# Kernel tuning notes

Measured on AMD Instinct MI355X. Metric: run time of the kernel, lower is better.

## Reference

```python
import jax, jax.numpy as jnp
import numpy as np

N = 50000      # nodes
E = 800000     # edges (avg degree 16)
DIN = 500      # input_dim
HID = 100      # hid_dim (fixed in module)
DOUT = 64      # output_dim
EPS = 1e-5     # LayerNorm eps (torch default)


def _layer_norm(x, g, b):
    mu = jnp.mean(x, axis=-1, keepdims=True)
    var = jnp.var(x, axis=-1, keepdims=True)
    return (x - mu) / jnp.sqrt(var + EPS) * g + b


def _gcn_conv(x, src, tgt, W, b):
    # PyG GCNConv: self-loops + symmetric normalization + linear + scatter-add
    h = x @ W  # [N, out]
    idx = jnp.arange(N)
    src_sl = jnp.concatenate([src, idx])
    tgt_sl = jnp.concatenate([tgt, idx])
    deg = jax.ops.segment_sum(jnp.ones(src_sl.shape, h.dtype), tgt_sl, num_segments=N)
    dinv = jnp.where(deg > 0, deg ** -0.5, 0.0)
    norm = dinv[src_sl] * dinv[tgt_sl]  # [E+N]
    out = jax.ops.segment_sum(h[src_sl] * norm[:, None], tgt_sl, num_segments=N)
    return out + b


def setup_inputs() -> dict:
    key = jax.random.key(0)
    ks = jax.random.split(key, 10)
    glorot = lambda k, fi, fo: jax.random.normal(k, (fi, fo), jnp.float32) * np.float32(1.0 / np.sqrt(fi))
    z = lambda d: jnp.zeros((d,), jnp.float32)
    return dict(
        data_x=jax.random.normal(ks[0], (N, DIN), jnp.float32),
        data_edge_index=jax.random.randint(ks[1], (2, E), 0, N),
        data_edge_attr=jnp.zeros((E,), jnp.int32),  # single relation type
        t_W1=glorot(ks[2], DIN, HID), t_b1=z(HID), t_g1=jnp.ones((HID,), jnp.float32), t_be1=z(HID),
        t_W2=glorot(ks[3], HID, HID), t_b2=z(HID), t_g2=jnp.ones((HID,), jnp.float32), t_be2=z(HID),
        r_Wrel=glorot(ks[4], HID, HID)[None],  # [n_relations=1, H, H]
        r_Wself=glorot(ks[5], HID, HID), r_b=z(HID),
        c1_W=glorot(ks[6], HID, HID), c1_b=z(HID),
        c2_W=glorot(ks[7], HID, DOUT), c2_b=z(DOUT),
    )


def reference(data_x, data_edge_index, data_edge_attr,
              t_W1, t_b1, t_g1, t_be1, t_W2, t_b2, t_g2, t_be2,
              r_Wrel, r_Wself, r_b, c1_W, c1_b, c2_W, c2_b):
    src, tgt = data_edge_index[0], data_edge_index[1]
    # transform: Linear -> LN -> ReLU -> Linear -> LN -> ReLU
    x = jax.nn.relu(_layer_norm(data_x @ t_W1 + t_b1, t_g1, t_be1))
    x = jax.nn.relu(_layer_norm(x @ t_W2 + t_b2, t_g2, t_be2))
    # RGCN, n_relations=1, n_layers=1: per-relation message + self transform
    msgs = x[src] @ r_Wrel[0]  # edge_attr is all relation 0
    x = x @ r_Wself + jax.ops.segment_sum(msgs, tgt, num_segments=N) + r_b
    x = jax.nn.relu(x)  # dropout = identity (eval)
    x = jax.nn.relu(_gcn_conv(x, src, tgt, c1_W, c1_b))
    x = _gcn_conv(x, src, tgt, c2_W, c2_b)
    return jax.nn.log_softmax(x, axis=1)
```

## Files before the change

kernel.cpp:

```cpp
#include <hip/hip_runtime.h>
#include <hip/hip_bf16.h>

typedef __attribute__((ext_vector_type(8))) short short8;
typedef __attribute__((ext_vector_type(8))) unsigned short ushort8;
typedef __attribute__((ext_vector_type(4))) float f32x4;

static constexpr int NN = 50000;
static constexpr int NE = 800000;
static constexpr int SCAN_B = 196;

#define MFMA16x16x32 __builtin_amdgcn_mfma_f32_16x16x32_bf16

__device__ __forceinline__ float b2f(unsigned short u){
  unsigned v = ((unsigned)u) << 16;
  return __builtin_bit_cast(float, v);
}
__device__ __forceinline__ unsigned short f2b(float f){
  unsigned x = __builtin_bit_cast(unsigned, f);
  unsigned r = (x + 0x7fffu + ((x >> 16) & 1u)) >> 16;
  return (unsigned short)r;
}

__device__ __align__(256) int   g_isf32;
__device__ __align__(256) unsigned short g_W1t  [112 * 512];
__device__ __align__(256) unsigned short g_W2t  [112 * 128];
__device__ __align__(256) unsigned short g_WselfT[112 * 128];
__device__ __align__(256) unsigned short g_WrelT [112 * 128];
__device__ __align__(256) unsigned short g_c1Wt [112 * 128];
__device__ __align__(256) unsigned short g_c2Wt [64 * 128];
__device__ __align__(256) unsigned short g_bufA[(size_t)NN * 128];
__device__ __align__(256) unsigned short g_bufB[(size_t)NN * 128];
__device__ __align__(256) unsigned short g_bufC[(size_t)NN * 128];
__device__ __align__(256) int   g_deg[NN];
__device__ __align__(256) int   g_rowptr[NN + 1];
__device__ __align__(256) int   g_cursor[NN];
__device__ __align__(256) int   g_colidx[NE];
__device__ __align__(256) float g_dinv[NN];
__device__ __align__(256) int   g_partial[256];

__device__ __forceinline__ float ld_in(const void* p, int idx, int isf32){
  if (isf32) return ((const float*)p)[idx];
  return b2f(((const unsigned short*)p)[idx]);
}

__global__ void k_detect_zero(const unsigned short* __restrict__ x){
  if (blockIdx.x == 0){
    __shared__ int sh[256];
    int tid = threadIdx.x;
    int cnt = 0;
    for (int j = 0; j < 16; j++){
      unsigned short h = x[(size_t)(tid * 16 + j) * 2];
      int e = (h >> 7) & 0xFF;
      if (e >= 90 && e <= 160) cnt++;
    }
    sh[tid] = cnt;
    __syncthreads();
    for (int off = 128; off > 0; off >>= 1){
      if (tid < off) sh[tid] += sh[tid + off];
      __syncthreads();
    }
    if (tid == 0) g_isf32 = (sh[0] < 2458) ? 1 : 0;
  } else {
    int i = (blockIdx.x - 1) * 256 + threadIdx.x;
    if (i < NN){ g_deg[i] = 0; g_cursor[i] = 0; }
  }
}

__device__ __forceinline__ void xp_one(const void* W, unsigned short* Wt, int idx,
                                       int K, int Nc, int Kpad, int isf32){
  int n = idx / Kpad;
  int k = idx - n * Kpad;
  float v = 0.f;
  if (n < Nc && k < K) v = ld_in(W, k * Nc + n, isf32);
  Wt[idx] = f2b(v);
}
__global__ void k_transpose_all(const void* W1, const void* W2, const void* Wself,
                                const void* Wrel, const void* c1W, const void* c2W){
  int idx = blockIdx.x * 256 + threadIdx.x;
  const int isf32 = g_isf32;
  if (idx < 57344){ xp_one(W1, g_W1t, idx, 500, 100, 512, isf32); return; }
  idx -= 57344;
  if (idx < 14336){ xp_one(W2,    g_W2t,    idx, 100, 100, 128, isf32); return; }
  idx -= 14336;
  if (idx < 14336){ xp_one(Wself, g_WselfT, idx, 100, 100, 128, isf32); return; }
  idx -= 14336;
  if (idx < 14336){ xp_one(Wrel,  g_WrelT,  idx, 100, 100, 128, isf32); return; }
  idx -= 14336;
  if (idx < 14336){ xp_one(c1W,   g_c1Wt,   idx, 100, 100, 128, isf32); return; }
  idx -= 14336;
  if (idx < 8192){  xp_one(c2W,   g_c2Wt,   idx, 100, 64,  128, isf32); }
}

__global__ void k_deg(const int* __restrict__ tgt){
  int e = blockIdx.x * 256 + threadIdx.x;
  if (e < NE) atomicAdd(&g_deg[tgt[e]], 1);
}
__global__ __launch_bounds__(256) void k_scan1(){
  __shared__ int sh[256];
  int t = threadIdx.x;
  int i = blockIdx.x * 256 + t;
  int val = (i < NN) ? g_deg[i] : 0;
  sh[t] = val; __syncthreads();
#pragma unroll
  for (int off = 1; off < 256; off <<= 1){
    int v = (t >= off) ? sh[t - off] : 0;
    __syncthreads(); sh[t] += v; __syncthreads();
  }
  if (i < NN){ g_rowptr[i] = sh[t] - val; g_dinv[i] = rsqrtf((float)(val + 1)); }
  if (t == 255) g_partial[blockIdx.x] = sh[255];
}
__global__ __launch_bounds__(256) void k_scan2(){
  __shared__ int sh[256];
  int t = threadIdx.x;
  int val = (t < SCAN_B) ? g_partial[t] : 0;
  sh[t] = val; __syncthreads();
#pragma unroll
  for (int off = 1; off < 256; off <<= 1){
    int v = (t >= off) ? sh[t - off] : 0;
    __syncthreads(); sh[t] += v; __syncthreads();
  }
  if (t < SCAN_B) g_partial[t] = sh[t] - val;
  if (t == 255) g_rowptr[NN] = sh[255];
}
__global__ __launch_bounds__(256) void k_scan3(){
  int i = blockIdx.x * 256 + threadIdx.x;
  if (i < NN) g_rowptr[i] += g_partial[blockIdx.x];
}
__global__ void k_fill(const int* __restrict__ src, const int* __restrict__ tgt){
  int e = blockIdx.x * 256 + threadIdx.x;
  if (e >= NE) return;
  int t = tgt[e];
  int pos = g_rowptr[t] + atomicAdd(&g_cursor[t], 1);
  g_colidx[pos] = src[e];
}


__device__ __forceinline__ void body_gemm1_compute(const void* Aext, int row0,
    int m, int q, int kbase, int isf32, f32x4* acc){
  if (isf32){
    const float* base = (const float*)Aext + (size_t)(row0 + m) * 500;
    f32x4 L[8];
#pragma unroll
    for (int c = 0; c < 4; c++){
      int col = kbase + c * 32 + q * 8;
      L[2 * c]     = *reinterpret_cast<const f32x4*>(base + min(col, 496));
      L[2 * c + 1] = *reinterpret_cast<const f32x4*>(base + min(col + 4, 496));
    }
#pragma unroll
    for (int c = 0; c < 4; c++){
      f32x4 lo = L[2 * c], hi = L[2 * c + 1];
      short8 a = {(short)f2b(lo[0]), (short)f2b(lo[1]), (short)f2b(lo[2]), (short)f2b(lo[3]),
                  (short)f2b(hi[0]), (short)f2b(hi[1]), (short)f2b(hi[2]), (short)f2b(hi[3])};
      const int k0 = kbase + c * 32 + q * 8;
#pragma unroll
      for (int t = 0; t < 7; t++){
        short8 b = *reinterpret_cast<const short8*>(g_W1t + (size_t)(t * 16 + m) * 512 + k0);
        acc[t] = MFMA16x16x32(a, b, acc[t], 0, 0, 0);
      }
    }
  } else {
    const unsigned short* base = (const unsigned short*)Aext + (size_t)(row0 + m) * 500;
    ushort4 U[8];
#pragma unroll
    for (int c = 0; c < 4; c++){
      int col = kbase + c * 32 + q * 8;
      U[2 * c]     = *reinterpret_cast<const ushort4*>(base + min(col, 496));
      U[2 * c + 1] = *reinterpret_cast<const ushort4*>(base + min(col + 4, 496));
    }
#pragma unroll
    for (int c = 0; c < 4; c++){
      ushort4 lo = U[2 * c], hi = U[2 * c + 1];
      short8 a = {(short)lo.x, (short)lo.y, (short)lo.z, (short)lo.w,
                  (short)hi.x, (short)hi.y, (short)hi.z, (short)hi.w};
      const int k0 = kbase + c * 32 + q * 8;
#pragma unroll
      for (int t = 0; t < 7; t++){
        short8 b = *reinterpret_cast<const short8*>(g_W1t + (size_t)(t * 16 + m) * 512 + k0);
        acc[t] = MFMA16x16x32(a, b, acc[t], 0, 0, 0);
      }
    }
  }
}

__device__ __forceinline__ short8 frag_from_lds(const float* xT, int m, int k0){
  const float* ax = xT + m * 132 + k0;
  short8 a = {(short)f2b(ax[0]), (short)f2b(ax[1]), (short)f2b(ax[2]), (short)f2b(ax[3]),
              (short)f2b(ax[4]), (short)f2b(ax[5]), (short)f2b(ax[6]), (short)f2b(ax[7])};
  return a;
}

__device__ __forceinline__ void epi_ln_to_lds(const float* red, float* xT,
    int lane, int m, int q, int isf32,
    const void* bias, const void* gamma, const void* beta){
  float bf_[7], gf_[7], ef_[7];
#pragma unroll
  for (int t = 0; t < 7; t++){
    int col = t * 16 + m;
    bool ok = col < 100;
    bf_[t] = ok ? ld_in(bias, col, isf32)  : 0.f;
    gf_[t] = ok ? ld_in(gamma, col, isf32) : 0.f;
    ef_[t] = ok ? ld_in(beta, col, isf32)  : 0.f;
  }
#pragma unroll
  for (int r = 0; r < 4; r++){
    float vals[7], s1 = 0.f, s2 = 0.f;
#pragma unroll
    for (int t = 0; t < 7; t++){
      const float* rv = &red[(t * 4 + r) * 256];
      float v = rv[lane] + rv[64 + lane] + rv[128 + lane] + rv[192 + lane];
      int col = t * 16 + m;
      v = (col < 100) ? (v + bf_[t]) : 0.f;
      vals[t] = v; s1 += v; s2 += v * v;
    }
#pragma unroll
    for (int msk = 1; msk < 16; msk <<= 1){
      s1 += __shfl_xor(s1, msk, 64);
      s2 += __shfl_xor(s2, msk, 64);
    }
    float mu = s1 * 0.01f;
    float var = fmaxf(s2 * 0.01f - mu * mu, 0.f);
    float rstd = rsqrtf(var + 1e-5f);
    float* xrow = xT + (q * 4 + r) * 132;
#pragma unroll
    for (int t = 0; t < 7; t++){
      int col = t * 16 + m;
      float y = fmaxf((vals[t] - mu) * rstd * gf_[t] + ef_[t], 0.f);
      xrow[col] = (col < 100) ? y : 0.f;
    }
    xrow[112 + m] = 0.f;
  }
}

__device__ __forceinline__ void epi_ln_to_global(const float* red, unsigned short* outb,
    int row0, int lane, int m, int q, int isf32,
    const void* bias, const void* gamma, const void* beta){
  float bf_[7], gf_[7], ef_[7];
#pragma unroll
  for (int t = 0; t < 7; t++){
    int col = t * 16 + m;
    bool ok = col < 100;
    bf_[t] = ok ? ld_in(bias, col, isf32)  : 0.f;
    gf_[t] = ok ? ld_in(gamma, col, isf32) : 0.f;
    ef_[t] = ok ? ld_in(beta, col, isf32)  : 0.f;
  }
#pragma unroll
  for (int r = 0; r < 4; r++){
    float vals[7], s1 = 0.f, s2 = 0.f;
#pragma unroll
    for (int t = 0; t < 7; t++){
      const float* rv = &red[(t * 4 + r) * 256];
      float v = rv[lane] + rv[64 + lane] + rv[128 + lane] + rv[192 + lane];
      int col = t * 16 + m;
      v = (col < 100) ? (v + bf_[t]) : 0.f;
      vals[t] = v; s1 += v; s2 += v * v;
    }
#pragma unroll
    for (int msk = 1; msk < 16; msk <<= 1){
      s1 += __shfl_xor(s1, msk, 64);
      s2 += __shfl_xor(s2, msk, 64);
    }
    float mu = s1 * 0.01f;
    float var = fmaxf(s2 * 0.01f - mu * mu, 0.f);
    float rstd = rsqrtf(var + 1e-5f);
    unsigned short* orow = outb + (size_t)(row0 + q * 4 + r) * 128;
#pragma unroll
    for (int t = 0; t < 7; t++){
      int col = t * 16 + m;
      float y = fmaxf((vals[t] - mu) * rstd * gf_[t] + ef_[t], 0.f);
      orow[col] = f2b((col < 100) ? y : 0.f);
    }
    orow[112 + m] = 0;
  }
}

__device__ __forceinline__ void epi_biasrelu_to_global(const float* red,
    unsigned short* outb, int row0, int lane, int m, int q, int isf32,
    const void* bias){
  float bf_[7];
#pragma unroll
  for (int t = 0; t < 7; t++){
    int col = t * 16 + m;
    bf_[t] = (col < 100) ? ld_in(bias, col, isf32) : 0.f;
  }
#pragma unroll
  for (int r = 0; r < 4; r++){
    unsigned short* orow = outb + (size_t)(row0 + q * 4 + r) * 128;
#pragma unroll
    for (int t = 0; t < 7; t++){
      const float* rv = &red[(t * 4 + r) * 256];
      float v = rv[lane] + rv[64 + lane] + rv[128 + lane] + rv[192 + lane];
      int col = t * 16 + m;
      float y = fmaxf(v + bf_[t], 0.f);
      orow[col] = f2b((col < 100) ? y : 0.f);
    }
    orow[112 + m] = 0;
  }
}

__device__ __forceinline__ void epi_biasrelu_to_lds(const float* red, float* xT,
    int lane, int m, int q, int isf32, const void* bias){
  float bf_[7];
#pragma unroll
  for (int t = 0; t < 7; t++){
    int col = t * 16 + m;
    bf_[t] = (col < 100) ? ld_in(bias, col, isf32) : 0.f;
  }
#pragma unroll
  for (int r = 0; r < 4; r++){
    float* xrow = xT + (q * 4 + r) * 132;
#pragma unroll
    for (int t = 0; t < 7; t++){
      const float* rv = &red[(t * 4 + r) * 256];
      float v = rv[lane] + rv[64 + lane] + rv[128 + lane] + rv[192 + lane];
      int col = t * 16 + m;
      float y = fmaxf(v + bf_[t], 0.f);
      xrow[col] = (col < 100) ? y : 0.f;
    }
    xrow[112 + m] = 0.f;
  }
}

template<int MODE>
__device__ __forceinline__ void agg_to_lds(int node, int nl, int c8, float* aggT){
  const unsigned short* x = (MODE == 1) ? g_bufC : g_bufB;
  float wt = (MODE != 0) ? g_dinv[node] : 1.f;
  float a[4][8];
#pragma unroll
  for (int j = 0; j < 4; j++)
#pragma unroll
    for (int k = 0; k < 8; k++) a[j][k] = 0.f;
  int p0 = g_rowptr[node], p1 = g_rowptr[node + 1];
  for (int p = p0; p < p1; p += 4){
    int sj[4]; float wj[4];
#pragma unroll
    for (int j = 0; j < 4; j++){
      bool ok = (p + j) < p1;
      sj[j] = ok ? g_colidx[p + j] : node;
      wj[j] = ok ? ((MODE != 0) ? g_dinv[sj[j]] * wt : 1.f) : 0.f;
    }
    ushort8 r[4];
#pragma unroll
    for (int j = 0; j < 4; j++)
      r[j] = *reinterpret_cast<const ushort8*>(&x[(size_t)sj[j] * 128 + c8]);
#pragma unroll
    for (int j = 0; j < 4; j++)
#pragma unroll
      for (int k = 0; k < 8; k++) a[j][k] += wj[j] * b2f((unsigned short)r[j][k]);
  }
  if (MODE != 0){
    float ws = wt * wt;
    ushort8 sv = *reinterpret_cast<const ushort8*>(&x[(size_t)node * 128 + c8]);
#pragma unroll
    for (int k = 0; k < 8; k++) a[0][k] += ws * b2f((unsigned short)sv[k]);
  }
  float* arow = aggT + nl * 132;
#pragma unroll
  for (int k = 0; k < 8; k++)
    arow[c8 + k] = a[0][k] + a[1][k] + a[2][k] + a[3][k];
}


__global__ __launch_bounds__(256, 4) void k_gemm12(const void* __restrict__ Aext,
    const void* b1, const void* gm1, const void* be1,
    const void* b2, const void* gm2, const void* be2){
  __shared__ float red[28 * 256];
  __shared__ float xT[16 * 132];
  const int tid = threadIdx.x;
  const int w = tid >> 6, lane = tid & 63;
  const int m = lane & 15, q = lane >> 4;
  const int row0 = blockIdx.x * 16;
  const int isf32 = g_isf32;

  f32x4 acc[7] = {};
  body_gemm1_compute(Aext, row0, m, q, w * 128, isf32, acc);
#pragma unroll
  for (int t = 0; t < 7; t++)
#pragma unroll
    for (int r = 0; r < 4; r++)
      red[(t * 4 + r) * 256 + tid] = acc[t][r];
  __syncthreads();
  if (w == 0) epi_ln_to_lds(red, xT, lane, m, q, isf32, b1, gm1, be1);
  __syncthreads();

  f32x4 acc2[7] = {};
  const int k0 = w * 32 + q * 8;
  {
    short8 a = frag_from_lds(xT, m, k0);
#pragma unroll
    for (int t = 0; t < 7; t++){
      short8 b = *reinterpret_cast<const short8*>(g_W2t + (size_t)(t * 16 + m) * 128 + k0);
      acc2[t] = MFMA16x16x32(a, b, acc2[t], 0, 0, 0);
    }
  }
#pragma unroll
  for (int t = 0; t < 7; t++)
#pragma unroll
    for (int r = 0; r < 4; r++)
      red[(t * 4 + r) * 256 + tid] = acc2[t][r];
  __syncthreads();
  if (w == 0) epi_ln_to_global(red, g_bufB, row0, lane, m, q, isf32, b2, gm2, be2);
}

__global__ __launch_bounds__(256, 4) void k_rgcn_f(const void* rb){
  __shared__ float red[28 * 256];
  __shared__ float aggT[16 * 132];
  const int tid = threadIdx.x;
  agg_to_lds<0>(blockIdx.x * 16 + (tid >> 4), tid >> 4, (tid & 15) * 8, aggT);
  __syncthreads();

  const int w = tid >> 6, lane = tid & 63;
  const int m = lane & 15, q = lane >> 4;
  const int row0 = blockIdx.x * 16;
  const int k0 = w * 32 + q * 8;
  f32x4 acc[7] = {};
  {
    short8 a1 = *reinterpret_cast<const short8*>(g_bufB + (size_t)(row0 + m) * 128 + k0);
#pragma unroll
    for (int t = 0; t < 7; t++){
      short8 b = *reinterpret_cast<const short8*>(g_WselfT + (size_t)(t * 16 + m) * 128 + k0);
      acc[t] = MFMA16x16x32(a1, b, acc[t], 0, 0, 0);
    }
    short8 a2 = frag_from_lds(aggT, m, k0);
#pragma unroll
    for (int t = 0; t < 7; t++){
      short8 b = *reinterpret_cast<const short8*>(g_WrelT + (size_t)(t * 16 + m) * 128 + k0);
      acc[t] = MFMA16x16x32(a2, b, acc[t], 0, 0, 0);
    }
  }
#pragma unroll
  for (int t = 0; t < 7; t++)
#pragma unroll
    for (int r = 0; r < 4; r++)
      red[(t * 4 + r) * 256 + tid] = acc[t][r];
  __syncthreads();
  if (w == 0) epi_biasrelu_to_global(red, g_bufC, row0, lane, m, q, g_isf32, rb);
}

__global__ __launch_bounds__(256, 4) void k_conv_f(const void* c1b){
  __shared__ float red[28 * 256];
  __shared__ float aggT[16 * 132];
  const int tid = threadIdx.x;
  agg_to_lds<1>(blockIdx.x * 16 + (tid >> 4), tid >> 4, (tid & 15) * 8, aggT);
  __syncthreads();

  const int w = tid >> 6, lane = tid & 63;
  const int m = lane & 15, q = lane >> 4;
  const int row0 = blockIdx.x * 16;
  const int k0 = w * 32 + q * 8;
  f32x4 acc[7] = {};
  {
    short8 a = frag_from_lds(aggT, m, k0);
#pragma unroll
    for (int t = 0; t < 7; t++){
      short8 b = *reinterpret_cast<const short8*>(g_c1Wt + (size_t)(t * 16 + m) * 128 + k0);
      acc[t] = MFMA16x16x32(a, b, acc[t], 0, 0, 0);
    }
  }
#pragma unroll
  for (int t = 0; t < 7; t++)
#pragma unroll
    for (int r = 0; r < 4; r++)
      red[(t * 4 + r) * 256 + tid] = acc[t][r];
  __syncthreads();
  if (w == 0) epi_biasrelu_to_lds(red, aggT, lane, m, q, g_isf32, c1b);
  __syncthreads();

  f32x4 acc2[4] = {};
  {
    short8 a = frag_from_lds(aggT, m, k0);
#pragma unroll
    for (int t = 0; t < 4; t++){
      short8 b = *reinterpret_cast<const short8*>(g_c2Wt + (size_t)(t * 16 + m) * 128 + k0);
      acc2[t] = MFMA16x16x32(a, b, acc2[t], 0, 0, 0);
    }
  }
#pragma unroll
  for (int t = 0; t < 4; t++)
#pragma unroll
    for (int r = 0; r < 4; r++)
      red[(t * 4 + r) * 256 + tid] = acc2[t][r];
  __syncthreads();
  if (w == 0){
#pragma unroll
    for (int r = 0; r < 4; r++){
      unsigned short* orow = g_bufA + (size_t)(row0 + q * 4 + r) * 64;
#pragma unroll
      for (int t = 0; t < 4; t++){
        const float* rv = &red[(t * 4 + r) * 256];
        float v = rv[lane] + rv[64 + lane] + rv[128 + lane] + rv[192 + lane];
        orow[t * 16 + m] = f2b(v);
      }
    }
  }
}

__global__ __launch_bounds__(256) void k_agg_lsm(const void* __restrict__ bias,
                                                 void* __restrict__ outv){
  const int isf32 = g_isf32;
  int node = blockIdx.x * 32 + (threadIdx.x >> 3);
  if (node >= NN) return;
  const int c8 = (threadIdx.x & 7) * 8;
  float wt = g_dinv[node];
  float a[4][8];
#pragma unroll
  for (int j = 0; j < 4; j++)
#pragma unroll
    for (int k = 0; k < 8; k++) a[j][k] = 0.f;
  int p0 = g_rowptr[node], p1 = g_rowptr[node + 1];
  for (int p = p0; p < p1; p += 4){
    int sj[4]; float wj[4];
#pragma unroll
    for (int j = 0; j < 4; j++){
      bool ok = (p + j) < p1;
      sj[j] = ok ? g_colidx[p + j] : node;
      wj[j] = ok ? g_dinv[sj[j]] * wt : 0.f;
    }
    ushort8 r[4];
#pragma unroll
    for (int j = 0; j < 4; j++)
      r[j] = *reinterpret_cast<const ushort8*>(&g_bufA[(size_t)sj[j] * 64 + c8]);
#pragma unroll
    for (int j = 0; j < 4; j++)
#pragma unroll
      for (int k = 0; k < 8; k++) a[j][k] += wj[j] * b2f((unsigned short)r[j][k]);
  }
  float ws = wt * wt;
  ushort8 sv = *reinterpret_cast<const ushort8*>(&g_bufA[(size_t)node * 64 + c8]);
#pragma unroll
  for (int k = 0; k < 8; k++) a[0][k] += ws * b2f((unsigned short)sv[k]);

  float v[8], mx = -1e30f;
#pragma unroll
  for (int k = 0; k < 8; k++){
    v[k] = a[0][k] + a[1][k] + a[2][k] + a[3][k] + ld_in(bias, c8 + k, isf32);
    mx = fmaxf(mx, v[k]);
  }
#pragma unroll
  for (int msk = 1; msk < 8; msk <<= 1) mx = fmaxf(mx, __shfl_xor(mx, msk, 64));
  float se = 0.f;
#pragma unroll
  for (int k = 0; k < 8; k++) se += expf(v[k] - mx);
#pragma unroll
  for (int msk = 1; msk < 8; msk <<= 1) se += __shfl_xor(se, msk, 64);
  float lse = logf(se);
  size_t ro = (size_t)node * 64 + c8;
  if (isf32){
    float* o = (float*)outv + ro;
#pragma unroll
    for (int k = 0; k < 8; k++) o[k] = v[k] - mx - lse;
  } else {
    unsigned short* o = (unsigned short*)outv + ro;
#pragma unroll
    for (int k = 0; k < 8; k++) o[k] = f2b(v[k] - mx - lse);
  }
}

extern "C" void kernel_launch(void* const* d_in, const int* in_sizes, int n_in,
                              void* d_out, int out_size, void* d_ws, size_t ws_size,
                              hipStream_t stream){
  (void)in_sizes; (void)n_in; (void)out_size; (void)d_ws; (void)ws_size;
  const void* data_x = d_in[0];
  const int* ei = (const int*)d_in[1];
  const int* src = ei;
  const int* tgt = ei + NE;
  const void *W1 = d_in[3], *b1 = d_in[4], *gm1 = d_in[5], *be1 = d_in[6];
  const void *W2 = d_in[7], *b2 = d_in[8], *gm2 = d_in[9], *be2 = d_in[10];
  const void *Wrel = d_in[11], *Wself = d_in[12], *rb = d_in[13];
  const void *c1W = d_in[14], *c1b = d_in[15];
  const void *c2W = d_in[16], *c2b = d_in[17];

  k_detect_zero<<<1 + (NN + 255) / 256, 256, 0, stream>>>((const unsigned short*)data_x);
  k_transpose_all<<<(122880 + 255) / 256, 256, 0, stream>>>(W1, W2, Wself, Wrel, c1W, c2W);

  k_deg<<<(NE + 255) / 256, 256, 0, stream>>>(tgt);
  k_scan1<<<SCAN_B, 256, 0, stream>>>();
  k_scan2<<<1, 256, 0, stream>>>();
  k_scan3<<<SCAN_B, 256, 0, stream>>>();
  k_fill<<<(NE + 255) / 256, 256, 0, stream>>>(src, tgt);

  k_gemm12<<<3125, 256, 0, stream>>>(data_x, b1, gm1, be1, b2, gm2, be2);
  k_rgcn_f<<<3125, 256, 0, stream>>>(rb);
  k_conv_f<<<3125, 256, 0, stream>>>(c1b);
  k_agg_lsm<<<(NN + 31) / 32, 256, 0, stream>>>(c2b, d_out);
}
```

Measured before the change: 487.3 us.

## Give each wave its own 16-row tile, dropping split-K LDS reduction

The three fused GEMM kernels now give each of the 4 waves its own 16-row tile and run the full K loop per wave, instead of splitting K across waves. This removes the 28x256 float LDS reduction buffer and the single-wave epilogue. Epilogues (bias, LayerNorm, ReLU) now run per wave directly on MFMA accumulators. Aggregation tiles are stored in LDS as bf16 rather than float, with 32 columns per thread and two neighbours per loop step. The block count drops to NBLK with row-bound guards, which adds register pressure per wave and changes the gather access pattern.

```diff
diff --git a/kernel.cpp b/kernel.cpp
--- a/kernel.cpp
+++ b/kernel.cpp
@@ -8,6 +8,7 @@
 static constexpr int NN = 50000;
 static constexpr int NE = 800000;
 static constexpr int SCAN_B = 196;
+static constexpr int NBLK = (NN + 63) / 64;
 
 #define MFMA16x16x32 __builtin_amdgcn_mfma_f32_16x16x32_bf16
 
@@ -19,6 +20,9 @@
   unsigned x = __builtin_bit_cast(unsigned, f);
   unsigned r = (x + 0x7fffu + ((x >> 16) & 1u)) >> 16;
   return (unsigned short)r;
+}
+__device__ __forceinline__ short8 u2s(ushort8 v){
+  return __builtin_bit_cast(short8, v);
 }
 
 __device__ __align__(256) int   g_isf32;
@@ -135,339 +139,235 @@
 }
 
 
-__device__ __forceinline__ void body_gemm1_compute(const void* Aext, int row0,
-    int m, int q, int kbase, int isf32, f32x4* acc){
-  if (isf32){
-    const float* base = (const float*)Aext + (size_t)(row0 + m) * 500;
-    f32x4 L[8];
-#pragma unroll
-    for (int c = 0; c < 4; c++){
-      int col = kbase + c * 32 + q * 8;
-      L[2 * c]     = *reinterpret_cast<const f32x4*>(base + min(col, 496));
-      L[2 * c + 1] = *reinterpret_cast<const f32x4*>(base + min(col + 4, 496));
-    }
-#pragma unroll
-    for (int c = 0; c < 4; c++){
-      f32x4 lo = L[2 * c], hi = L[2 * c + 1];
-      short8 a = {(short)f2b(lo[0]), (short)f2b(lo[1]), (short)f2b(lo[2]), (short)f2b(lo[3]),
-                  (short)f2b(hi[0]), (short)f2b(hi[1]), (short)f2b(hi[2]), (short)f2b(hi[3])};
-      const int k0 = kbase + c * 32 + q * 8;
-#pragma unroll
-      for (int t = 0; t < 7; t++){
-        short8 b = *reinterpret_cast<const short8*>(g_W1t + (size_t)(t * 16 + m) * 512 + k0);
-        acc[t] = MFMA16x16x32(a, b, acc[t], 0, 0, 0);
-      }
-    }
-  } else {
-    const unsigned short* base = (const unsigned short*)Aext + (size_t)(row0 + m) * 500;
-    ushort4 U[8];
-#pragma unroll
-    for (int c = 0; c < 4; c++){
-      int col = kbase + c * 32 + q * 8;
-      U[2 * c]     = *reinterpret_cast<const ushort4*>(base + min(col, 496));
-      U[2 * c + 1] = *reinterpret_cast<const ushort4*>(base + min(col + 4, 496));
-    }
-#pragma unroll
-    for (int c = 0; c < 4; c++){
-      ushort4 lo = U[2 * c], hi = U[2 * c + 1];
-      short8 a = {(short)lo.x, (short)lo.y, (short)lo.z, (short)lo.w,
-                  (short)hi.x, (short)hi.y, (short)hi.z, (short)hi.w};
-      const int k0 = kbase + c * 32 + q * 8;
-#pragma unroll
-      for (int t = 0; t < 7; t++){
-        short8 b = *reinterpret_cast<const short8*>(g_W1t + (size_t)(t * 16 + m) * 512 + k0);
-        acc[t] = MFMA16x16x32(a, b, acc[t], 0, 0, 0);
-      }
-    }
-  }
-}
-
-__device__ __forceinline__ short8 frag_from_lds(const float* xT, int m, int k0){
-  const float* ax = xT + m * 132 + k0;
-  short8 a = {(short)f2b(ax[0]), (short)f2b(ax[1]), (short)f2b(ax[2]), (short)f2b(ax[3]),
-              (short)f2b(ax[4]), (short)f2b(ax[5]), (short)f2b(ax[6]), (short)f2b(ax[7])};
-  return a;
-}
-
-__device__ __forceinline__ void epi_ln_to_lds(const float* red, float* xT,
-    int lane, int m, int q, int isf32,
-    const void* bias, const void* gamma, const void* beta){
+template<int DO_LN>
+__device__ __forceinline__ void wave_epi(const f32x4* acc, unsigned short* dst,
+    int rstride, int grow0, int lane, int isf32,
+    const void* bias, const void* gm, const void* be){
+  const int m = lane & 15;
+  const int q = lane >> 4;
   float bf_[7], gf_[7], ef_[7];
 #pragma unroll
   for (int t = 0; t < 7; t++){
     int col = t * 16 + m;
     bool ok = col < 100;
-    bf_[t] = ok ? ld_in(bias, col, isf32)  : 0.f;
-    gf_[t] = ok ? ld_in(gamma, col, isf32) : 0.f;
-    ef_[t] = ok ? ld_in(beta, col, isf32)  : 0.f;
+    bf_[t] = ok ? ld_in(bias, col, isf32) : 0.f;
+    if (DO_LN){
+      gf_[t] = ok ? ld_in(gm, col, isf32) : 0.f;
+      ef_[t] = ok ? ld_in(be, col, isf32) : 0.f;
+    }
   }
 #pragma unroll
   for (int r = 0; r < 4; r++){
+    int rl = q * 4 + r;
     float vals[7], s1 = 0.f, s2 = 0.f;
-#pragma unroll
-    for (int t = 0; t < 7; t++){
-      const float* rv = &red[(t * 4 + r) * 256];
-      float v = rv[lane] + rv[64 + lane] + rv[128 + lane] + rv[192 + lane];
-      int col = t * 16 + m;
-      v = (col < 100) ? (v + bf_[t]) : 0.f;
-      vals[t] = v; s1 += v; s2 += v * v;
-    }
-#pragma unroll
-    for (int msk = 1; msk < 16; msk <<= 1){
-      s1 += __shfl_xor(s1, msk, 64);
-      s2 += __shfl_xor(s2, msk, 64);
-    }
-    float mu = s1 * 0.01f;
-    float var = fmaxf(s2 * 0.01f - mu * mu, 0.f);
-    float rstd = rsqrtf(var + 1e-5f);
-    float* xrow = xT + (q * 4 + r) * 132;
 #pragma unroll
     for (int t = 0; t < 7; t++){
       int col = t * 16 + m;
-      float y = fmaxf((vals[t] - mu) * rstd * gf_[t] + ef_[t], 0.f);
-      xrow[col] = (col < 100) ? y : 0.f;
-    }
-    xrow[112 + m] = 0.f;
-  }
-}
-
-__device__ __forceinline__ void epi_ln_to_global(const float* red, unsigned short* outb,
-    int row0, int lane, int m, int q, int isf32,
-    const void* bias, const void* gamma, const void* beta){
-  float bf_[7], gf_[7], ef_[7];
-#pragma unroll
-  for (int t = 0; t < 7; t++){
-    int col = t * 16 + m;
-    bool ok = col < 100;
-    bf_[t] = ok ? ld_in(bias, col, isf32)  : 0.f;
-    gf_[t] = ok ? ld_in(gamma, col, isf32) : 0.f;
-    ef_[t] = ok ? ld_in(beta, col, isf32)  : 0.f;
-  }
-#pragma unroll
-  for (int r = 0; r < 4; r++){
-    float vals[7], s1 = 0.f, s2 = 0.f;
-#pragma unroll
-    for (int t = 0; t < 7; t++){
-      const float* rv = &red[(t * 4 + r) * 256];
-      float v = rv[lane] + rv[64 + lane] + rv[128 + lane] + rv[192 + lane];
-      int col = t * 16 + m;
-      v = (col < 100) ? (v + bf_[t]) : 0.f;
+      float v = (col < 100) ? (acc[t][r] + bf_[t]) : 0.f;
       vals[t] = v; s1 += v; s2 += v * v;
     }
-#pragma unroll
-    for (int msk = 1; msk < 16; msk <<= 1){
-      s1 += __shfl_xor(s1, msk, 64);
-      s2 += __shfl_xor(s2, msk, 64);
-    }
-    float mu = s1 * 0.01f;
-    float var = fmaxf(s2 * 0.01f - mu * mu, 0.f);
-    float rstd = rsqrtf(var + 1e-5f);
-    unsigned short* orow = outb + (size_t)(row0 + q * 4 + r) * 128;
-#pragma unroll
-    for (int t = 0; t < 7; t++){
-      int col = t * 16 + m;
-      float y = fmaxf((vals[t] - mu) * rstd * gf_[t] + ef_[t], 0.f);
-      orow[col] = f2b((col < 100) ? y : 0.f);
-    }
-    orow[112 + m] = 0;
-  }
-}
-
-__device__ __forceinline__ void epi_biasrelu_to_global(const float* red,
-    unsigned short* outb, int row0, int lane, int m, int q, int isf32,
-    const void* bias){
-  float bf_[7];
-#pragma unroll
-  for (int t = 0; t < 7; t++){
-    int col = t * 16 + m;
-    bf_[t] = (col < 100) ? ld_in(bias, col, isf32) : 0.f;
-  }
-#pragma unroll
-  for (int r = 0; r < 4; r++){
-    unsigned short* orow = outb + (size_t)(row0 + q * 4 + r) * 128;
-#pragma unroll
-    for (int t = 0; t < 7; t++){
-      const float* rv = &red[(t * 4 + r) * 256];
-      float v = rv[lane] + rv[64 + lane] + rv[128 + lane] + rv[192 + lane];
-      int col = t * 16 + m;
-      float y = fmaxf(v + bf_[t], 0.f);
-      orow[col] = f2b((col < 100) ? y : 0.f);
-    }
-    orow[112 + m] = 0;
-  }
-}
-
-__device__ __forceinline__ void epi_biasrelu_to_lds(const float* red, float* xT,
-    int lane, int m, int q, int isf32, const void* bias){
-  float bf_[7];
-#pragma unroll
-  for (int t = 0; t < 7; t++){
-    int col = t * 16 + m;
-    bf_[t] = (col < 100) ? ld_in(bias, col, isf32) : 0.f;
-  }
-#pragma unroll
-  for (int r = 0; r < 4; r++){
-    float* xrow = xT + (q * 4 + r) * 132;
-#pragma unroll
-    for (int t = 0; t < 7; t++){
-      const float* rv = &red[(t * 4 + r) * 256];
-      float v = rv[lane] + rv[64 + lane] + rv[128 + lane] + rv[192 + lane];
-      int col = t * 16 + m;
-      float y = fmaxf(v + bf_[t], 0.f);
-      xrow[col] = (col < 100) ? y : 0.f;
-    }
-    xrow[112 + m] = 0.f;
+    if (DO_LN){
+#pragma unroll
+      for (int msk = 1; msk < 16; msk <<= 1){
+        s1 += __shfl_xor(s1, msk, 64);
+        s2 += __shfl_xor(s2, msk, 64);
+      }
+      float mu = s1 * 0.01f;
+      float var = fmaxf(s2 * 0.01f - mu * mu, 0.f);
+      float rstd = rsqrtf(var + 1e-5f);
+#pragma unroll
+      for (int t = 0; t < 7; t++)
+        vals[t] = (vals[t] - mu) * rstd * gf_[t] + ef_[t];
+    }
+    if (grow0 + rl < NN){
+      unsigned short* orow = dst + (size_t)rl * rstride;
+#pragma unroll
+      for (int t = 0; t < 7; t++){
+        int col = t * 16 + m;
+        float y = fmaxf(vals[t], 0.f);
+        orow[col] = f2b((col < 100) ? y : 0.f);
+      }
+      orow[112 + m] = 0;
+    }
   }
 }
 
 template<int MODE>
-__device__ __forceinline__ void agg_to_lds(int node, int nl, int c8, float* aggT){
-  const unsigned short* x = (MODE == 1) ? g_bufC : g_bufB;
-  float wt = (MODE != 0) ? g_dinv[node] : 1.f;
-  float a[4][8];
-#pragma unroll
-  for (int j = 0; j < 4; j++)
-#pragma unroll
-    for (int k = 0; k < 8; k++) a[j][k] = 0.f;
-  int p0 = g_rowptr[node], p1 = g_rowptr[node + 1];
-  for (int p = p0; p < p1; p += 4){
-    int sj[4]; float wj[4];
-#pragma unroll
-    for (int j = 0; j < 4; j++){
-      bool ok = (p + j) < p1;
-      sj[j] = ok ? g_colidx[p + j] : node;
-      wj[j] = ok ? ((MODE != 0) ? g_dinv[sj[j]] * wt : 1.f) : 0.f;
-    }
-    ushort8 r[4];
-#pragma unroll
-    for (int j = 0; j < 4; j++)
-      r[j] = *reinterpret_cast<const ushort8*>(&x[(size_t)sj[j] * 128 + c8]);
-#pragma unroll
-    for (int j = 0; j < 4; j++)
-#pragma unroll
-      for (int k = 0; k < 8; k++) a[j][k] += wj[j] * b2f((unsigned short)r[j][k]);
+__device__ __forceinline__ void agg_tile(const unsigned short* __restrict__ x,
+    unsigned short* aggT, int tid, int brow0){
+  const int nl = tid >> 2;
+  const int c0 = (tid & 3) * 32;
+  const int node = min(brow0 + nl, NN - 1);
+  const float wt = (MODE != 0) ? g_dinv[node] : 1.f;
+  float a[32];
+#pragma unroll
+  for (int k = 0; k < 32; k++) a[k] = 0.f;
+  const int p0 = g_rowptr[node], p1 = g_rowptr[node + 1];
+  for (int p = p0; p < p1; p += 2){
+    int s0 = g_colidx[p];
+    bool ok1 = (p + 1) < p1;
+    int s1 = ok1 ? g_colidx[p + 1] : node;
+    float w0 = (MODE != 0) ? g_dinv[s0] * wt : 1.f;
+    float w1 = ok1 ? ((MODE != 0) ? g_dinv[s1] * wt : 1.f) : 0.f;
+    ushort8 r0[4], r1[4];
+#pragma unroll
+    for (int u = 0; u < 4; u++){
+      r0[u] = *reinterpret_cast<const ushort8*>(&x[(size_t)s0 * 128 + c0 + u * 8]);
+      r1[u] = *reinterpret_cast<const ushort8*>(&x[(size_t)s1 * 128 + c0 + u * 8]);
+    }
+#pragma unroll
+    for (int u = 0; u < 4; u++)
+#pragma unroll
+      for (int k = 0; k < 8; k++){
+        a[u * 8 + k] += w0 * b2f((unsigned short)r0[u][k]);
+        a[u * 8 + k] += w1 * b2f((unsigned short)r1[u][k]);
+      }
   }
   if (MODE != 0){
     float ws = wt * wt;
-    ushort8 sv = *reinterpret_cast<const ushort8*>(&x[(size_t)node * 128 + c8]);
-#pragma unroll
-    for (int k = 0; k < 8; k++) a[0][k] += ws * b2f((unsigned short)sv[k]);
-  }
-  float* arow = aggT + nl * 132;
-#pragma unroll
-  for (int k = 0; k < 8; k++)
-    arow[c8 + k] = a[0][k] + a[1][k] + a[2][k] + a[3][k];
+#pragma unroll
+    for (int u = 0; u < 4; u++){
+      ushort8 sv = *reinterpret_cast<const ushort8*>(&x[(size_t)node * 128 + c0 + u * 8]);
+#pragma unroll
+      for (int k = 0; k < 8; k++) a[u * 8 + k] += ws * b2f((unsigned short)sv[k]);
+    }
+  }
+  unsigned short* arow = aggT + nl * 136 + c0;
+#pragma unroll
+  for (int u = 0; u < 4; u++){
+    ushort8 o;
+#pragma unroll
+    for (int k = 0; k < 8; k++) o[k] = f2b(a[u * 8 + k]);
+    *reinterpret_cast<ushort8*>(&arow[u * 8]) = o;
+  }
 }
 
 
 __global__ __launch_bounds__(256, 4) void k_gemm12(const void* __restrict__ Aext,
     const void* b1, const void* gm1, const void* be1,
     const void* b2, const void* gm2, const void* be2){
-  __shared__ float red[28 * 256];
-  __shared__ float xT[16 * 132];
+  __shared__ unsigned short xT[4][16][136];
   const int tid = threadIdx.x;
   const int w = tid >> 6, lane = tid & 63;
   const int m = lane & 15, q = lane >> 4;
-  const int row0 = blockIdx.x * 16;
+  const int row0 = blockIdx.x * 64 + w * 16;
   const int isf32 = g_isf32;
+  const int arow = min(row0 + m, NN - 1);
 
   f32x4 acc[7] = {};
-  body_gemm1_compute(Aext, row0, m, q, w * 128, isf32, acc);
-#pragma unroll
-  for (int t = 0; t < 7; t++)
-#pragma unroll
-    for (int r = 0; r < 4; r++)
-      red[(t * 4 + r) * 256 + tid] = acc[t][r];
+  if (isf32){
+    const float* base = (const float*)Aext + (size_t)arow * 500;
+#pragma unroll 4
+    for (int kc = 0; kc < 16; kc++){
+      int col = kc * 32 + q * 8;
+      f32x4 lo = *reinterpret_cast<const f32x4*>(base + min(col, 496));
+      f32x4 hi = *reinterpret_cast<const f32x4*>(base + min(col + 4, 496));
+      short8 a = {(short)f2b(lo[0]), (short)f2b(lo[1]), (short)f2b(lo[2]), (short)f2b(lo[3]),
+                  (short)f2b(hi[0]), (short)f2b(hi[1]), (short)f2b(hi[2]), (short)f2b(hi[3])};
+#pragma unroll
+      for (int t = 0; t < 7; t++){
+        short8 b = *reinterpret_cast<const short8*>(g_W1t + (size_t)(t * 16 + m) * 512 + col);
+        acc[t] = MFMA16x16x32(a, b, acc[t], 0, 0, 0);
+      }
+    }
+  } else {
+    const unsigned short* base = (const unsigned short*)Aext + (size_t)arow * 500;
+#pragma unroll 4
+    for (int kc = 0; kc < 16; kc++){
+      int col = kc * 32 + q * 8;
+      ushort4 lo = *reinterpret_cast<const ushort4*>(base + min(col, 496));
+      ushort4 hi = *reinterpret_cast<const ushort4*>(base + min(col + 4, 496));
+      short8 a = {(short)lo.x, (short)lo.y, (short)lo.z, (short)lo.w,
+                  (short)hi.x, (short)hi.y, (short)hi.z, (short)hi.w};
+#pragma unroll
+      for (int t = 0; t < 7; t++){
+        short8 b = *reinterpret_cast<const short8*>(g_W1t + (size_t)(t * 16 + m) * 512 + col);
+        acc[t] = MFMA16x16x32(a, b, acc[t], 0, 0, 0);
+      }
+    }
+  }
+  wave_epi<1>(acc, &xT[w][0][0], 136, 0, lane, isf32, b1, gm1, be1);
   __syncthreads();
-  if (w == 0) epi_ln_to_lds(red, xT, lane, m, q, isf32, b1, gm1, be1);
-  __syncthreads();
 
   f32x4 acc2[7] = {};
-  const int k0 = w * 32 + q * 8;
-  {
-    short8 a = frag_from_lds(xT, m, k0);
+#pragma unroll
+  for (int kc = 0; kc < 4; kc++){
+    int k0 = kc * 32 + q * 8;
+    short8 a = u2s(*reinterpret_cast<const ushort8*>(&xT[w][m][k0]));
 #pragma unroll
     for (int t = 0; t < 7; t++){
       short8 b = *reinterpret_cast<const short8*>(g_W2t + (size_t)(t * 16 + m) * 128 + k0);
       acc2[t] = MFMA16x16x32(a, b, acc2[t], 0, 0, 0);
     }
   }
-#pragma unroll
-  for (int t = 0; t < 7; t++)
-#pragma unroll
-    for (int r = 0; r < 4; r++)
-      red[(t * 4 + r) * 256 + tid] = acc2[t][r];
-  __syncthreads();
-  if (w == 0) epi_ln_to_global(red, g_bufB, row0, lane, m, q, isf32, b2, gm2, be2);
+  wave_epi<1>(acc2, g_bufB + (size_t)row0 * 128, 128, row0, lane, isf32, b2, gm2, be2);
 }
 
 __global__ __launch_bounds__(256, 4) void k_rgcn_f(const void* rb){
-  __shared__ float red[28 * 256];
-  __shared__ float aggT[16 * 132];
+  __shared__ unsigned short aggT[64 * 136];
   const int tid = threadIdx.x;
-  agg_to_lds<0>(blockIdx.x * 16 + (tid >> 4), tid >> 4, (tid & 15) * 8, aggT);
+  const int brow0 = blockIdx.x * 64;
+  agg_tile<0>(g_bufB, aggT, tid, brow0);
   __syncthreads();
 
   const int w = tid >> 6, lane = tid & 63;
   const int m = lane & 15, q = lane >> 4;
-  const int row0 = blockIdx.x * 16;
-  const int k0 = w * 32 + q * 8;
+  const int row0 = brow0 + w * 16;
+  const int arow = min(row0 + m, NN - 1);
+  const int isf32 = g_isf32;
   f32x4 acc[7] = {};
-  {
-    short8 a1 = *reinterpret_cast<const short8*>(g_bufB + (size_t)(row0 + m) * 128 + k0);
+#pragma unroll
+  for (int kc = 0; kc < 4; kc++){
+    int k0 = kc * 32 + q * 8;
+    short8 a1 = u2s(*reinterpret_cast<const ushort8*>(&g_bufB[(size_t)arow * 128 + k0]));
 #pragma unroll
     for (int t = 0; t < 7; t++){
       short8 b = *reinterpret_cast<const short8*>(g_WselfT + (size_t)(t * 16 + m) * 128 + k0);
       acc[t] = MFMA16x16x32(a1, b, acc[t], 0, 0, 0);
     }
-    short8 a2 = frag_from_lds(aggT, m, k0);
+    short8 a2 = u2s(*reinterpret_cast<const ushort8*>(&aggT[(w * 16 + m) * 136 + k0]));
 #pragma unroll
     for (int t = 0; t < 7; t++){
       short8 b = *reinterpret_cast<const short8*>(g_WrelT + (size_t)(t * 16 + m) * 128 + k0);
       acc[t] = MFMA16x16x32(a2, b, acc[t], 0, 0, 0);
     }
   }
-#pragma unroll
-  for (int t = 0; t < 7; t++)
-#pragma unroll
-    for (int r = 0; r < 4; r++)
-      red[(t * 4 + r) * 256 + tid] = acc[t][r];
-  __syncthreads();
-  if (w == 0) epi_biasrelu_to_global(red, g_bufC, row0, lane, m, q, g_isf32, rb);
+  wave_epi<0>(acc, g_bufC + (size_t)row0 * 128, 128, row0, lane, isf32, rb, nullptr, nullptr);
 }
 
 __global__ __launch_bounds__(256, 4) void k_conv_f(const void* c1b){
-  __shared__ float red[28 * 256];
-  __shared__ float aggT[16 * 132];
+  __shared__ unsigned short aggT[64 * 136];
   const int tid = threadIdx.x;
-  agg_to_lds<1>(blockIdx.x * 16 + (tid >> 4), tid >> 4, (tid & 15) * 8, aggT);
+  const int brow0 = blockIdx.x * 64;
+  agg_tile<1>(g_bufC, aggT, tid, brow0);
   __syncthreads();
 
   const int w = tid >> 6, lane = tid & 63;
   const int m = lane & 15, q = lane >> 4;
-  const int row0 = blockIdx.x * 16;
-  const int k0 = w * 32 + q * 8;
+  const int row0 = brow0 + w * 16;
+  const int isf32 = g_isf32;
+  unsigned short* tile = aggT + w * 16 * 136;
+
   f32x4 acc[7] = {};
-  {
-    short8 a = frag_from_lds(aggT, m, k0);
+#pragma unroll
+  for (int kc = 0; kc < 4; kc++){
+    int k0 = kc * 32 + q * 8;
+    short8 a = u2s(*reinterpret_cast<const ushort8*>(&tile[m * 136 + k0]));
 #pragma unroll
     for (int t = 0; t < 7; t++){
       short8 b = *reinterpret_cast<const short8*>(g_c1Wt + (size_t)(t * 16 + m) * 128 + k0);
       acc[t] = MFMA16x16x32(a, b, acc[t], 0, 0, 0);
     }
   }
-#pragma unroll
-  for (int t = 0; t < 7; t++)
-#pragma unroll
-    for (int r = 0; r < 4; r++)
-      red[(t * 4 + r) * 256 + tid] = acc[t][r];
   __syncthreads();
-  if (w == 0) epi_biasrelu_to_lds(red, aggT, lane, m, q, g_isf32, c1b);
+  wave_epi<0>(acc, tile, 136, 0, lane, isf32, c1b, nullptr, nullptr);
   __syncthreads();
 
   f32x4 acc2[4] = {};
-  {
-    short8 a = frag_from_lds(aggT, m, k0);
+#pragma unroll
+  for (int kc = 0; kc < 4; kc++){
+    int k0 = kc * 32 + q * 8;
+    short8 a = u2s(*reinterpret_cast<const ushort8*>(&tile[m * 136 + k0]));
 #pragma unroll
     for (int t = 0; t < 4; t++){
       short8 b = *reinterpret_cast<const short8*>(g_c2Wt + (size_t)(t * 16 + m) * 128 + k0);
@@ -475,21 +375,12 @@
     }
   }
 #pragma unroll
-  for (int t = 0; t < 4; t++)
-#pragma unroll
-    for (int r = 0; r < 4; r++)
-      red[(t * 4 + r) * 256 + tid] = acc2[t][r];
-  __syncthreads();
-  if (w == 0){
-#pragma unroll
-    for (int r = 0; r < 4; r++){
-      unsigned short* orow = g_bufA + (size_t)(row0 + q * 4 + r) * 64;
-#pragma unroll
-      for (int t = 0; t < 4; t++){
-        const float* rv = &red[(t * 4 + r) * 256];
-        float v = rv[lane] + rv[64 + lane] + rv[128 + lane] + rv[192 + lane];
-        orow[t * 16 + m] = f2b(v);
-      }
+  for (int r = 0; r < 4; r++){
+    int row = row0 + q * 4 + r;
+    if (row < NN){
+      unsigned short* orow = g_bufA + (size_t)row * 64;
+#pragma unroll
+      for (int t = 0; t < 4; t++) orow[t * 16 + m] = f2b(acc2[t][r]);
     }
   }
 }
@@ -578,8 +469,8 @@
   k_scan3<<<SCAN_B, 256, 0, stream>>>();
   k_fill<<<(NE + 255) / 256, 256, 0, stream>>>(src, tgt);
 
-  k_gemm12<<<3125, 256, 0, stream>>>(data_x, b1, gm1, be1, b2, gm2, be2);
-  k_rgcn_f<<<3125, 256, 0, stream>>>(rb);
-  k_conv_f<<<3125, 256, 0, stream>>>(c1b);
+  k_gemm12<<<NBLK, 256, 0, stream>>>(data_x, b1, gm1, be1, b2, gm2, be2);
+  k_rgcn_f<<<NBLK, 256, 0, stream>>>(rb);
+  k_conv_f<<<NBLK, 256, 0, stream>>>(c1b);
   k_agg_lsm<<<(NN + 31) / 32, 256, 0, stream>>>(c2b, d_out);
 }
```

After: 480.9 us. Within noise of the previous version (-1.3%).
